# Performance work log

Hardware: AMD Instinct MI355X
Metric: run time of the kernel (lower is better)

The kernel has to match this reference:

```python
import jax, jax.numpy as jnp
import numpy as np

N_NODES = 50000
N_EDGES = 800000
IN_CH = 256
OUT_CH = 128
HID = 2 * OUT_CH  # 256
LN_EPS = 1e-5


def _add_self_loops(edge_index, n):
    loop = jnp.arange(n, dtype=edge_index.dtype)
    src = jnp.concatenate([edge_index[0], loop])
    dst = jnp.concatenate([edge_index[1], loop])
    return src, dst


def _gcn_norm(src, dst, n):
    # PyG GCNConv norm: deg over source index, symmetric normalization
    ones = jnp.ones(src.shape[0], dtype=jnp.float32)
    deg = jax.ops.segment_sum(ones, src, num_segments=n)
    dinv = jnp.where(deg > 0, deg ** -0.5, 0.0)
    return dinv[src] * dinv[dst]  # [E+N]


def _gcn_conv(x, src, dst, norm, w, b, gamma=None, beta=None):
    h = x @ w                              # [N, out]
    msgs = norm[:, None] * h[src]          # gather + scale, [E+N, out]
    out = jax.ops.segment_sum(msgs, dst, num_segments=x.shape[0])
    if gamma is not None:
        out = gamma * out + beta           # FiLM modulation (per-feature)
    return out + b


def _layernorm(x):
    mu = jnp.mean(x, axis=-1, keepdims=True)
    var = jnp.var(x, axis=-1, keepdims=True)
    return (x - mu) * jax.lax.rsqrt(var + LN_EPS)


def setup_inputs() -> dict:
    key = jax.random.key(0)
    ks = jax.random.split(key, 20)

    def g(k, shape, scale=0.05):
        return jax.random.normal(k, shape, dtype=jnp.float32) * scale

    x = jax.random.normal(ks[0], (N_NODES, IN_CH), dtype=jnp.float32)
    edge_index = jax.random.randint(ks[1], (2, N_EDGES), 0, N_NODES, dtype=jnp.int64)
    return {
        "x": x,
        "edge_index": edge_index,
        "conv1_w": g(ks[2], (IN_CH, HID)),
        "conv1_b": g(ks[3], (HID,)),
        "conv2_w": g(ks[4], (HID, OUT_CH)),
        "conv2_b": g(ks[5], (OUT_CH,)),
        "sig_conv_w": g(ks[6], (IN_CH, HID)),
        "sig_conv_b": g(ks[7], (HID,)),
        "fc1_w": g(ks[8], (HID, HID)),
        "fc1_b": g(ks[9], (HID,)),
        "fc2_w": g(ks[10], (HID, HID)),
        "fc2_b": g(ks[11], (HID,)),
        "fc3_w": g(ks[12], (OUT_CH, HID)),
        "fc3_b": g(ks[13], (OUT_CH,)),
        "fc4_w": g(ks[14], (OUT_CH, HID)),
        "fc4_b": g(ks[15], (OUT_CH,)),
    }


def reference(x, edge_index, conv1_w, conv1_b, conv2_w, conv2_b,
              sig_conv_w, sig_conv_b, fc1_w, fc1_b, fc2_w, fc2_b,
              fc3_w, fc3_b, fc4_w, fc4_b):
    n = x.shape[0]
    src, dst = _add_self_loops(edge_index, n)
    norm = _gcn_norm(src, dst, n)

    # --- GraphSignature (use_gcn_sig=True) ---
    s = jax.nn.relu(_gcn_conv(x, src, dst, norm, sig_conv_w, sig_conv_b))
    s = s.sum(0)  # [HID]
    gamma1 = jnp.tanh(s @ fc1_w.T + fc1_b)  # [HID]
    beta1 = jnp.tanh(s @ fc2_w.T + fc2_b)   # [HID]
    gamma2 = jnp.tanh(s @ fc3_w.T + fc3_b)  # [OUT]
    beta2 = jnp.tanh(s @ fc4_w.T + fc4_b)   # [OUT]

    # inner_loop=True: signature outputs are detached
    gamma1, beta1, gamma2, beta2 = map(jax.lax.stop_gradient,
                                       (gamma1, beta1, gamma2, beta2))

    # --- Encoder (GAE) ---
    h = jax.nn.relu(_gcn_conv(x, src, dst, norm, conv1_w, conv1_b,
                              gamma=gamma1, beta=beta1))
    h = _layernorm(h)
    out = _gcn_conv(h, src, dst, norm, conv2_w, conv2_b,
                    gamma=gamma2, beta=beta2)
    out = _layernorm(out)
    return out
```

## Files before the change

kernel.cpp:

```cpp
#include <hip/hip_runtime.h>

typedef _Float16 f16;
typedef f16 f16x8 __attribute__((ext_vector_type(8)));
typedef float f32x4 __attribute__((ext_vector_type(4)));
typedef unsigned short u16;
typedef unsigned int u32;

#define IN_CH  256
#define HID    256
#define OUT_CH 128
#define LN_EPS 1e-5f
#define NSLOT  32
#define NR     4
#define NC     64
#define RS     12544
#define HT     512


__global__ __launch_bounds__(HT) void k_hist(const int* __restrict__ ei, int nE, int nN,
                                             int* __restrict__ hP) {
    __shared__ int h[RS];
    int r = blockIdx.x & (NR - 1), c = blockIdx.x >> 2;
    int rsz = (nN + NR - 1) / NR;
    int r0 = r * rsz;
    int sz = nN - r0; if (sz > rsz) sz = rsz;
    for (int i = threadIdx.x; i < sz; i += HT) h[i] = 0;
    __syncthreads();
    int nT = nE + nN;
    int chunk = (nT + NC - 1) / NC;
    int e0 = c * chunk, e1 = e0 + chunk; if (e1 > nT) e1 = nT;
    for (int eb = e0 + (int)threadIdx.x; eb < e1; eb += HT * 4) {
        int ss[4], dd[4];
        #pragma unroll
        for (int u = 0; u < 4; u++) {
            int e = eb + u * HT;
            ss[u] = -1; dd[u] = -1;
            if (e < e1) {
                if (e < nE) { ss[u] = ei[e]; dd[u] = ei[nE + e]; }
                else { ss[u] = e - nE; dd[u] = e - nE; }
            }
        }
        #pragma unroll
        for (int u = 0; u < 4; u++) {
            if ((unsigned)(ss[u] - r0) < (unsigned)sz) atomicAdd(&h[ss[u] - r0], 1);
            if ((unsigned)(dd[u] - r0) < (unsigned)sz) atomicAdd(&h[dd[u] - r0], 0x10000);
        }
    }
    __syncthreads();
    for (int i = threadIdx.x; i < sz; i += HT) hP[(size_t)c * nN + r0 + i] = h[i];
}


__global__ __launch_bounds__(256) void k_alloc(const int* __restrict__ hP,
                                               int* __restrict__ rowstart,
                                               int* __restrict__ chunkbase,
                                               int* __restrict__ cnt_tot,
                                               float* __restrict__ dinv,
                                               int* __restrict__ ctr, int nN,
                                               const float* __restrict__ x, f16* __restrict__ xh,
                                               int nelem, int nAllocB, int nCast,
                                               const float* __restrict__ sigw,
                                               const float* __restrict__ c1w,
                                               const float* __restrict__ c2w,
                                               f16* __restrict__ Wt1, f16* __restrict__ Wt2) {
    int bid = blockIdx.x;
    if (bid < nAllocB) {
        int i = bid * 256 + threadIdx.x;
        int lane = threadIdx.x & 63;
        int cnt = 0, dg = 0;
        if (i < nN) {
            for (int c = 0; c < NC; c++) {
                unsigned pk = (unsigned)hP[(size_t)c * nN + i];
                cnt += (int)(pk >> 16);
                dg  += (int)(pk & 0xffffu);
            }
        }
        int p = cnt;
        #pragma unroll
        for (int off = 1; off < 64; off <<= 1) {
            int v = __shfl_up(p, off, 64);
            if (lane >= off) p += v;
        }
        int tot = __shfl(p, 63, 64);
        int base = 0;
        if (lane == 0) base = atomicAdd(ctr, tot);
        base = __shfl(base, 0, 64);
        if (i < nN) {
            int nb = base + p - cnt;
            rowstart[i] = nb;
            cnt_tot[i] = cnt;
            dinv[i] = rsqrtf((float)dg);
            int run = nb;
            for (int c = 0; c < NC; c++) {
                chunkbase[(size_t)c * nN + i] = run;
                run += (int)((unsigned)hP[(size_t)c * nN + i] >> 16);
            }
        }
    } else if (bid < nAllocB + nCast) {
        int i = (bid - nAllocB) * 2048 + threadIdx.x * 8;
        if (i >= nelem) return;
        float4 a = *(const float4*)(x + i);
        float4 b = *(const float4*)(x + i + 4);
        f16x8 o = { (f16)a.x, (f16)a.y, (f16)a.z, (f16)a.w,
                    (f16)b.x, (f16)b.y, (f16)b.z, (f16)b.w };
        *(f16x8*)(xh + i) = o;
    } else {
        int i = (bid - nAllocB - nCast) * 256 + threadIdx.x;
        if (i < 512 * 256) {
            int n = i >> 8, k = i & 255;
            float v = (n < 256) ? sigw[k * 256 + n] : c1w[k * 256 + (n - 256)];
            Wt1[(size_t)n * 256 + k] = (f16)v;
        } else {
            int j = i - 512 * 256;
            if (j < 128 * 256) {
                int n = j >> 8, k = j & 255;
                Wt2[(size_t)n * 256 + k] = (f16)c2w[k * 128 + n];
            }
        }
    }
}


__global__ __launch_bounds__(HT) void k_fill(const int* __restrict__ ei, int nE, int nN,
                                             const int* __restrict__ chunkbase,
                                             u16* __restrict__ src_sorted) {
    __shared__ int pos_[RS];
    int r = blockIdx.x & (NR - 1), c = blockIdx.x >> 2;
    int rsz = (nN + NR - 1) / NR;
    int r0 = r * rsz;
    int sz = nN - r0; if (sz > rsz) sz = rsz;
    for (int i = threadIdx.x; i < sz; i += HT)
        pos_[i] = chunkbase[(size_t)c * nN + r0 + i];
    __syncthreads();
    int nT = nE + nN;
    int chunk = (nT + NC - 1) / NC;
    int e0 = c * chunk, e1 = e0 + chunk; if (e1 > nT) e1 = nT;
    for (int eb = e0 + (int)threadIdx.x; eb < e1; eb += HT * 4) {
        int ss[4], dd[4];
        #pragma unroll
        for (int u = 0; u < 4; u++) {
            int e = eb + u * HT;
            ss[u] = -1; dd[u] = -1;
            if (e < e1) {
                if (e < nE) { ss[u] = ei[e]; dd[u] = ei[nE + e]; }
                else { ss[u] = e - nE; dd[u] = e - nE; }
            }
        }
        #pragma unroll
        for (int u = 0; u < 4; u++) {
            int l = dd[u] - r0;
            if ((unsigned)l < (unsigned)sz) {
                int pos = atomicAdd(&pos_[l], 1);
                src_sorted[pos] = (u16)ss[u];
            }
        }
    }
}


__global__ __launch_bounds__(256) void k_aggX(const f16* __restrict__ xh,
                                              const int* __restrict__ rowstart,
                                              const int* __restrict__ counts,
                                              const u16* __restrict__ srcs,
                                              const float* __restrict__ dinv,
                                              f16* __restrict__ AX, int nN) {
    int wv = threadIdx.x >> 6;
    int lane = threadIdx.x & 63;
    int node = blockIdx.x * 4 + wv;
    if (node >= nN) return;
    int h = lane >> 5, sub = lane & 31;
    int beg = rowstart[node];
    int cnt = counts[node];
    float acc0[8] = {}, acc1[8] = {};
    for (int base = 0; base < cnt; base += 64) {
        int el = base + lane;
        int sv = 0; float dv = 0.f;
        if (el < cnt) { sv = srcs[beg + el]; dv = dinv[sv]; }
        int rem = cnt - base; if (rem > 64) rem = 64;
        for (int e = 0; e < rem; e += 8) {
            int i0 = e + h, i1 = e + 2 + h, i2 = e + 4 + h, i3 = e + 6 + h;
            int sa = __shfl(sv, i0, 64), sb = __shfl(sv, i1, 64);
            int sc = __shfl(sv, i2, 64), sd = __shfl(sv, i3, 64);
            float na = __shfl(dv, i0, 64), nb = __shfl(dv, i1, 64);
            float nc = __shfl(dv, i2, 64), nd = __shfl(dv, i3, 64);
            if (i0 >= rem) na = 0.f;
            if (i1 >= rem) nb = 0.f;
            if (i2 >= rem) nc = 0.f;
            if (i3 >= rem) nd = 0.f;
            f16x8 va = *(const f16x8*)(xh + (size_t)sa * 256 + sub * 8);
            f16x8 vb = *(const f16x8*)(xh + (size_t)sb * 256 + sub * 8);
            f16x8 vc = *(const f16x8*)(xh + (size_t)sc * 256 + sub * 8);
            f16x8 vd = *(const f16x8*)(xh + (size_t)sd * 256 + sub * 8);
            #pragma unroll
            for (int j = 0; j < 8; j++) {
                acc0[j] = fmaf(na, (float)va[j], acc0[j]);
                acc1[j] = fmaf(nb, (float)vb[j], acc1[j]);
                acc0[j] = fmaf(nc, (float)vc[j], acc0[j]);
                acc1[j] = fmaf(nd, (float)vd[j], acc1[j]);
            }
        }
    }
    float dn = dinv[node];
    #pragma unroll
    for (int j = 0; j < 8; j++) {
        acc0[j] += acc1[j];
        acc0[j] += __shfl_xor(acc0[j], 32, 64);
    }
    if (lane < 32) {
        f16x8 o;
        #pragma unroll
        for (int j = 0; j < 8; j++) o[j] = (f16)(acc0[j] * dn);
        *(f16x8*)(AX + (size_t)node * 256 + sub * 8) = o;
    }
}


__global__ __launch_bounds__(256) void k_gemm_sig(const f16* __restrict__ AX,
                                                  const f16* __restrict__ Wt,
                                                  const float* __restrict__ sigb,
                                                  float* __restrict__ sig_part, int M) {
    __shared__ f16 tile[32][264];
    int t = threadIdx.x;
    int w = t >> 6, lane = t & 63, quad = lane >> 4, l16 = lane & 15;
    int m0 = blockIdx.x * 32;
    int cb = w * 64;
    f32x4 acc[2][4] = {};
    for (int kk = 0; kk < 256; kk += 32) {
        int ka = kk + quad * 8;
        f16x8 a[2];
        #pragma unroll
        for (int ms = 0; ms < 2; ms++) {
            int row = m0 + ms * 16 + l16; if (row >= M) row = M - 1;
            a[ms] = *(const f16x8*)(AX + (size_t)row * 256 + ka);
        }
        #pragma unroll
        for (int ns = 0; ns < 4; ns++) {
            f16x8 b = *(const f16x8*)(Wt + (size_t)(cb + ns * 16 + l16) * 256 + ka);
            acc[0][ns] = __builtin_amdgcn_mfma_f32_16x16x32_f16(a[0], b, acc[0][ns], 0, 0, 0);
            acc[1][ns] = __builtin_amdgcn_mfma_f32_16x16x32_f16(a[1], b, acc[1][ns], 0, 0, 0);
        }
    }
    #pragma unroll
    for (int ms = 0; ms < 2; ms++)
        #pragma unroll
        for (int ns = 0; ns < 4; ns++)
            #pragma unroll
            for (int r = 0; r < 4; r++) {
                int mr = ms * 16 + quad * 4 + r;
                int c = cb + ns * 16 + l16;
                float v = fmaxf(acc[ms][ns][r] + sigb[c], 0.f);
                if (m0 + mr >= M) v = 0.f;
                tile[mr][c] = (f16)v;
            }
    __syncthreads();
    float s = 0.f;
    #pragma unroll 8
    for (int r = 0; r < 32; r++) s += (float)tile[r][t];
    atomicAdd(&sig_part[(blockIdx.x & (NSLOT - 1)) * 256 + t], s);
}


__global__ __launch_bounds__(256) void k_fc(const float* __restrict__ sig_part,
                                            const float* __restrict__ f1w, const float* __restrict__ f1b,
                                            const float* __restrict__ f2w, const float* __restrict__ f2b,
                                            const float* __restrict__ f3w, const float* __restrict__ f3b,
                                            const float* __restrict__ f4w, const float* __restrict__ f4b,
                                            const float* __restrict__ c1b, const float* __restrict__ c2b,
                                            float* __restrict__ g1, float* __restrict__ bc1,
                                            float* __restrict__ g2, float* __restrict__ bc2) {
    __shared__ float ss[256];
    int t = threadIdx.x;
    float s = 0.f;
    for (int k = 0; k < NSLOT; k++) s += sig_part[k * 256 + t];
    ss[t] = s;
    __syncthreads();
    int wv = t >> 6, lane = t & 63;
    float s0 = ss[lane], s1 = ss[lane + 64], s2v = ss[lane + 128], s3 = ss[lane + 192];
    #pragma unroll
    for (int rr = 0; rr < 16; rr++) {
        int row = blockIdx.x * 64 + wv * 16 + rr;
        const float* w; const float* bb; const float* ex; float* dst; int r;
        if (row < 256)      { w = f1w; bb = f1b; dst = g1;  ex = 0;   r = row; }
        else if (row < 512) { w = f2w; bb = f2b; dst = bc1; ex = c1b; r = row - 256; }
        else if (row < 640) { w = f3w; bb = f3b; dst = g2;  ex = 0;   r = row - 512; }
        else                { w = f4w; bb = f4b; dst = bc2; ex = c2b; r = row - 640; }
        const float* wr = w + (size_t)r * 256;
        float a = wr[lane] * s0;
        a = fmaf(wr[lane + 64], s1, a);
        a = fmaf(wr[lane + 128], s2v, a);
        a = fmaf(wr[lane + 192], s3, a);
        #pragma unroll
        for (int off = 1; off < 64; off <<= 1) a += __shfl_xor(a, off, 64);
        if (lane == 0) dst[r] = tanhf(a + bb[r]) + (ex ? ex[r] : 0.f);
    }
}


__global__ __launch_bounds__(256) void k_c1f(const f16* __restrict__ AX,
                                             const f16* __restrict__ Wt,
                                             const f16* __restrict__ Wt2,
                                             const float* __restrict__ g1,
                                             const float* __restrict__ bc1,
                                             const float* __restrict__ dinv,
                                             f16* __restrict__ HW, int M) {
    __shared__ f16 ht[32][264];
    __shared__ float ps[32][5], ps2[32][5];
    __shared__ float mu_[32], rr_[32], sdinv[32];
    int t = threadIdx.x;
    int w = t >> 6, lane = t & 63, quad = lane >> 4, l16 = lane & 15;
    int m0 = blockIdx.x * 32;
    int cb = w * 64;
    f32x4 acc[2][4] = {};
    for (int kk = 0; kk < 256; kk += 32) {
        int ka = kk + quad * 8;
        f16x8 a[2];
        #pragma unroll
        for (int ms = 0; ms < 2; ms++) {
            int row = m0 + ms * 16 + l16; if (row >= M) row = M - 1;
            a[ms] = *(const f16x8*)(AX + (size_t)row * 256 + ka);
        }
        #pragma unroll
        for (int ns = 0; ns < 4; ns++) {
            f16x8 b = *(const f16x8*)(Wt + (size_t)(cb + ns * 16 + l16) * 256 + ka);
            acc[0][ns] = __builtin_amdgcn_mfma_f32_16x16x32_f16(a[0], b, acc[0][ns], 0, 0, 0);
            acc[1][ns] = __builtin_amdgcn_mfma_f32_16x16x32_f16(a[1], b, acc[1][ns], 0, 0, 0);
        }
    }

    float rs[2][4] = {{0.f,0.f,0.f,0.f},{0.f,0.f,0.f,0.f}};
    float rs2[2][4] = {{0.f,0.f,0.f,0.f},{0.f,0.f,0.f,0.f}};
    #pragma unroll
    for (int ns = 0; ns < 4; ns++) {
        int c = cb + ns * 16 + l16;
        float gv = g1[c], bv = bc1[c];
        #pragma unroll
        for (int ms = 0; ms < 2; ms++)
            #pragma unroll
            for (int r = 0; r < 4; r++) {
                float v = fmaxf(fmaf(gv, acc[ms][ns][r], bv), 0.f);
                acc[ms][ns][r] = v;
                rs[ms][r] += v;
                rs2[ms][r] = fmaf(v, v, rs2[ms][r]);
            }
    }
    #pragma unroll
    for (int off = 1; off < 16; off <<= 1)
        #pragma unroll
        for (int ms = 0; ms < 2; ms++)
            #pragma unroll
            for (int r = 0; r < 4; r++) {
                rs[ms][r]  += __shfl_xor(rs[ms][r], off, 64);
                rs2[ms][r] += __shfl_xor(rs2[ms][r], off, 64);
            }
    if (l16 == 0) {
        #pragma unroll
        for (int ms = 0; ms < 2; ms++)
            #pragma unroll
            for (int r = 0; r < 4; r++) {
                int mr = ms * 16 + quad * 4 + r;
                ps[mr][w] = rs[ms][r];
                ps2[mr][w] = rs2[ms][r];
            }
    }
    __syncthreads();
    if (t < 32) {
        float S = ps[t][0] + ps[t][1] + ps[t][2] + ps[t][3];
        float S2 = ps2[t][0] + ps2[t][1] + ps2[t][2] + ps2[t][3];
        float mu = S * (1.f / 256.f);
        mu_[t] = mu;
        rr_[t] = rsqrtf(S2 * (1.f / 256.f) - mu * mu + LN_EPS);
        int m = m0 + t;
        sdinv[t] = (m < M) ? dinv[m] : 0.f;
    }
    __syncthreads();
    #pragma unroll
    for (int ms = 0; ms < 2; ms++)
        #pragma unroll
        for (int r = 0; r < 4; r++) {
            int mr = ms * 16 + quad * 4 + r;
            float mu = mu_[mr], rr = rr_[mr];
            #pragma unroll
            for (int ns = 0; ns < 4; ns++)
                ht[mr][cb + ns * 16 + l16] = (f16)((acc[ms][ns][r] - mu) * rr);
        }
    __syncthreads();
    int cb2 = w * 32;
    f32x4 acc2[2][2] = {};
    for (int kk = 0; kk < 256; kk += 32) {
        int ka = kk + quad * 8;
        f16x8 a[2];
        #pragma unroll
        for (int ms = 0; ms < 2; ms++)
            a[ms] = *(const f16x8*)(&ht[ms * 16 + l16][ka]);
        #pragma unroll
        for (int ns = 0; ns < 2; ns++) {
            f16x8 b = *(const f16x8*)(Wt2 + (size_t)(cb2 + ns * 16 + l16) * 256 + ka);
            acc2[0][ns] = __builtin_amdgcn_mfma_f32_16x16x32_f16(a[0], b, acc2[0][ns], 0, 0, 0);
            acc2[1][ns] = __builtin_amdgcn_mfma_f32_16x16x32_f16(a[1], b, acc2[1][ns], 0, 0, 0);
        }
    }
    #pragma unroll
    for (int ms = 0; ms < 2; ms++)
        #pragma unroll
        for (int ns = 0; ns < 2; ns++)
            #pragma unroll
            for (int r = 0; r < 4; r++) {
                int mr = ms * 16 + quad * 4 + r;
                int m = m0 + mr;
                if (m < M) HW[(size_t)m * 128 + cb2 + ns * 16 + l16] = (f16)(acc2[ms][ns][r] * sdinv[mr]);
            }
}


__global__ __launch_bounds__(256) void k_agg2(const f16* __restrict__ HW,
                                              const int* __restrict__ rowstart,
                                              const int* __restrict__ counts,
                                              const u16* __restrict__ srcs,
                                              const float* __restrict__ dinv,
                                              const float* __restrict__ g2,
                                              const float* __restrict__ bc2,
                                              float* __restrict__ out, int nN) {
    int wv = threadIdx.x >> 6;
    int lane = threadIdx.x & 63;
    int node = blockIdx.x * 4 + wv;
    if (node >= nN) return;
    int q = lane >> 4, sub = lane & 15;
    int beg = rowstart[node];
    int cnt = counts[node];
    float acc0[8] = {}, acc1[8] = {};
    for (int base = 0; base < cnt; base += 64) {
        int el = base + lane;
        int sv = 0; float dv = 0.f;
        if (el < cnt) { sv = srcs[beg + el]; dv = 1.f; }
        int rem = cnt - base; if (rem > 64) rem = 64;
        for (int e = 0; e < rem; e += 8) {
            int i0 = e + q, i1 = e + 4 + q;
            int sa = __shfl(sv, i0, 64), sb = __shfl(sv, i1, 64);
            float na = __shfl(dv, i0, 64), nb = __shfl(dv, i1, 64);
            if (i0 >= rem) na = 0.f;
            if (i1 >= rem) nb = 0.f;
            f16x8 va = *(const f16x8*)(HW + (size_t)sa * 128 + sub * 8);
            f16x8 vb = *(const f16x8*)(HW + (size_t)sb * 128 + sub * 8);
            #pragma unroll
            for (int j = 0; j < 8; j++) {
                acc0[j] = fmaf(na, (float)va[j], acc0[j]);
                acc1[j] = fmaf(nb, (float)vb[j], acc1[j]);
            }
        }
    }
    float dn = dinv[node];
    #pragma unroll
    for (int j = 0; j < 8; j++) {
        acc0[j] += acc1[j];
        acc0[j] += __shfl_xor(acc0[j], 16, 64);
        acc0[j] += __shfl_xor(acc0[j], 32, 64);
    }
    int ch = sub * 8;
    float vfin[8];
    float s = 0.f, s2 = 0.f;
    #pragma unroll
    for (int j = 0; j < 8; j++) {
        float v = fmaf(g2[ch + j], acc0[j] * dn, bc2[ch + j]);
        vfin[j] = v;
        s += v; s2 = fmaf(v, v, s2);
    }
    #pragma unroll
    for (int off = 1; off < 16; off <<= 1) {
        s += __shfl_xor(s, off, 64);
        s2 += __shfl_xor(s2, off, 64);
    }
    float mu = s * (1.f / 128.f);
    float rr = rsqrtf(s2 * (1.f / 128.f) - mu * mu + LN_EPS);
    if (q == 0) {
        float4 o0 = { (vfin[0] - mu) * rr, (vfin[1] - mu) * rr,
                      (vfin[2] - mu) * rr, (vfin[3] - mu) * rr };
        float4 o1 = { (vfin[4] - mu) * rr, (vfin[5] - mu) * rr,
                      (vfin[6] - mu) * rr, (vfin[7] - mu) * rr };
        float* dst = out + (size_t)node * 128 + ch;
        *(float4*)dst = o0;
        *(float4*)(dst + 4) = o1;
    }
}


extern "C" void kernel_launch(void* const* d_in, const int* in_sizes, int n_in,
                              void* d_out, int out_size, void* d_ws, size_t ws_size,
                              hipStream_t stream) {
    const float* x    = (const float*)d_in[0];
    const int*   ei   = (const int*)d_in[1];
    const float* c1w  = (const float*)d_in[2];
    const float* c1b  = (const float*)d_in[3];
    const float* c2w  = (const float*)d_in[4];
    const float* c2b  = (const float*)d_in[5];
    const float* sigw = (const float*)d_in[6];
    const float* sigb = (const float*)d_in[7];
    const float* f1w  = (const float*)d_in[8];
    const float* f1b  = (const float*)d_in[9];
    const float* f2w  = (const float*)d_in[10];
    const float* f2b  = (const float*)d_in[11];
    const float* f3w  = (const float*)d_in[12];
    const float* f3b  = (const float*)d_in[13];
    const float* f4w  = (const float*)d_in[14];
    const float* f4b  = (const float*)d_in[15];
    float* out = (float*)d_out;

    int nN = in_sizes[0] / IN_CH;
    int nE = in_sizes[1] / 2;
    int nT = nE + nN;

    char* base = (char*)d_ws;
    size_t off = 0;
    auto alloc = [&](size_t bytes) { size_t o = off; off += (bytes + 255) & ~(size_t)255; return o; };

    size_t o_spart  = alloc((size_t)NSLOT * 256 * 4);
    size_t o_ctr    = alloc(256);
    size_t zero_bytes = off;
    size_t o_hP     = alloc((size_t)NC * nN * 4);
    size_t o_cbase  = alloc((size_t)NC * nN * 4);
    size_t o_g1     = alloc(256 * 4);
    size_t o_b1     = alloc(256 * 4);
    size_t o_g2     = alloc(128 * 4);
    size_t o_b2     = alloc(128 * 4);
    size_t o_rowst  = alloc((size_t)nN * 4);
    size_t o_cntt   = alloc((size_t)nN * 4);
    size_t o_dinv   = alloc((size_t)nN * 4);
    size_t o_src    = alloc((size_t)nT * 2);
    size_t o_wt1    = alloc(512 * 256 * 2);
    size_t o_wt2    = alloc(128 * 256 * 2);
    size_t o_xh     = alloc((size_t)nN * 256 * 2);
    size_t o_AX     = alloc((size_t)nN * 256 * 2);
    size_t o_HW     = alloc((size_t)nN * 128 * 2);

    float* spart  = (float*)(base + o_spart);
    int*   ctr    = (int*)(base + o_ctr);
    int*   hP     = (int*)(base + o_hP);
    int*   cbase  = (int*)(base + o_cbase);
    float* g1     = (float*)(base + o_g1);
    float* bc1    = (float*)(base + o_b1);
    float* g2     = (float*)(base + o_g2);
    float* bc2    = (float*)(base + o_b2);
    int*   rowst  = (int*)(base + o_rowst);
    int*   cntt   = (int*)(base + o_cntt);
    float* dinv   = (float*)(base + o_dinv);
    u16*   srcs   = (u16*)(base + o_src);
    f16*   Wt1    = (f16*)(base + o_wt1);
    f16*   Wt2    = (f16*)(base + o_wt2);
    f16*   xh     = (f16*)(base + o_xh);
    f16*   AX     = (f16*)(base + o_AX);
    f16*   HW     = (f16*)(base + o_HW);

    hipMemsetAsync(base, 0, zero_bytes, stream);

    k_hist<<<NR * NC, HT, 0, stream>>>(ei, nE, nN, hP);

    int nAllocB = (nN + 255) / 256;
    int nCast = (nN * IN_CH + 2047) / 2048;
    int nPrep = (512 * 256 + 128 * 256) / 256;
    k_alloc<<<nAllocB + nCast + nPrep, 256, 0, stream>>>(hP, rowst, cbase, cntt, dinv, ctr, nN,
                                                         x, xh, nN * IN_CH, nAllocB, nCast,
                                                         sigw, c1w, c2w, Wt1, Wt2);

    k_fill<<<NR * NC, HT, 0, stream>>>(ei, nE, nN, cbase, srcs);

    int nb4 = (nN + 3) / 4;
    int mg = (nN + 31) / 32;
    k_aggX<<<nb4, 256, 0, stream>>>(xh, rowst, cntt, srcs, dinv, AX, nN);
    k_gemm_sig<<<mg, 256, 0, stream>>>(AX, Wt1, sigb, spart, nN);
    k_fc<<<12, 256, 0, stream>>>(spart, f1w, f1b, f2w, f2b, f3w, f3b, f4w, f4b,
                                 c1b, c2b, g1, bc1, g2, bc2);
    k_c1f<<<mg, 256, 0, stream>>>(AX, Wt1 + 256 * 256, Wt2, g1, bc1, dinv, HW, nN);
    k_agg2<<<nb4, 256, 0, stream>>>(HW, rowst, cntt, srcs, dinv, g2, bc2, out, nN);
}
```

Baseline: 365.1 us.

## Pre-swizzle GEMM weights into MFMA fragment order and unroll gather loops deeper

Weight prep now stores the transposed f16 weights in MFMA B-fragment order, so each lane's 16-byte B load in the three GEMM kernels reads one contiguous, coalesced chunk instead of strided rows. The prep grid shrinks because each thread now writes eight values. The two aggregation kernels gain a 16-edge main loop that issues eight (or four) independent row gathers before accumulating, which raises memory-level parallelism at the cost of more registers. The old 8-edge loop remains as the tail.

```diff
diff --git a/kernel.cpp b/kernel.cpp
--- a/kernel.cpp
+++ b/kernel.cpp
@@ -106,16 +106,32 @@
         *(f16x8*)(xh + i) = o;
     } else {
         int i = (bid - nAllocB - nCast) * 256 + threadIdx.x;
-        if (i < 512 * 256) {
-            int n = i >> 8, k = i & 255;
-            float v = (n < 256) ? sigw[k * 256 + n] : c1w[k * 256 + (n - 256)];
-            Wt1[(size_t)n * 256 + k] = (f16)v;
+        if (i < 16384) {
+            int ct = i >> 9;
+            int rem = i & 511;
+            int kx = rem >> 6;
+            int lane = rem & 63;
+            int q = lane >> 4, l = lane & 15;
+            int n = (ct & 15) * 16 + l;
+            int k0 = kx * 32 + q * 8;
+            const float* src = (ct < 16) ? sigw : c1w;
+            f16x8 o;
+            #pragma unroll
+            for (int j = 0; j < 8; j++) o[j] = (f16)src[(size_t)(k0 + j) * 256 + n];
+            *(f16x8*)(Wt1 + (size_t)i * 8) = o;
         } else {
-            int j = i - 512 * 256;
-            if (j < 128 * 256) {
-                int n = j >> 8, k = j & 255;
-                Wt2[(size_t)n * 256 + k] = (f16)c2w[k * 128 + n];
-            }
+            int h = i - 16384;
+            int ct = h >> 9;
+            int rem = h & 511;
+            int kx = rem >> 6;
+            int lane = rem & 63;
+            int q = lane >> 4, l = lane & 15;
+            int n = ct * 16 + l;
+            int k0 = kx * 32 + q * 8;
+            f16x8 o;
+            #pragma unroll
+            for (int j = 0; j < 8; j++) o[j] = (f16)c2w[(size_t)(k0 + j) * 128 + n];
+            *(f16x8*)(Wt2 + (size_t)h * 8) = o;
         }
     }
 }
@@ -177,7 +193,28 @@
         int sv = 0; float dv = 0.f;
         if (el < cnt) { sv = srcs[beg + el]; dv = dinv[sv]; }
         int rem = cnt - base; if (rem > 64) rem = 64;
-        for (int e = 0; e < rem; e += 8) {
+        int e = 0;
+        for (; e + 16 <= rem; e += 16) {
+            int s_[8]; float n_[8];
+            #pragma unroll
+            for (int u = 0; u < 8; u++) {
+                int ii = e + u * 2 + h;
+                s_[u] = __shfl(sv, ii, 64);
+                n_[u] = __shfl(dv, ii, 64);
+            }
+            f16x8 v_[8];
+            #pragma unroll
+            for (int u = 0; u < 8; u++)
+                v_[u] = *(const f16x8*)(xh + (size_t)s_[u] * 256 + sub * 8);
+            #pragma unroll
+            for (int u = 0; u < 8; u++)
+                #pragma unroll
+                for (int j = 0; j < 8; j++) {
+                    float* a = (u & 1) ? acc1 : acc0;
+                    a[j] = fmaf(n_[u], (float)v_[u][j], a[j]);
+                }
+        }
+        for (; e < rem; e += 8) {
             int i0 = e + h, i1 = e + 2 + h, i2 = e + 4 + h, i3 = e + 6 + h;
             int sa = __shfl(sv, i0, 64), sb = __shfl(sv, i1, 64);
             int sc = __shfl(sv, i2, 64), sd = __shfl(sv, i3, 64);
@@ -225,8 +262,8 @@
     int m0 = blockIdx.x * 32;
     int cb = w * 64;
     f32x4 acc[2][4] = {};
-    for (int kk = 0; kk < 256; kk += 32) {
-        int ka = kk + quad * 8;
+    for (int kx = 0; kx < 8; kx++) {
+        int ka = kx * 32 + quad * 8;
         f16x8 a[2];
         #pragma unroll
         for (int ms = 0; ms < 2; ms++) {
@@ -235,7 +272,8 @@
         }
         #pragma unroll
         for (int ns = 0; ns < 4; ns++) {
-            f16x8 b = *(const f16x8*)(Wt + (size_t)(cb + ns * 16 + l16) * 256 + ka);
+            int ct = w * 4 + ns;
+            f16x8 b = *(const f16x8*)(Wt + ((size_t)((ct * 8 + kx) * 64 + lane) << 3));
             acc[0][ns] = __builtin_amdgcn_mfma_f32_16x16x32_f16(a[0], b, acc[0][ns], 0, 0, 0);
             acc[1][ns] = __builtin_amdgcn_mfma_f32_16x16x32_f16(a[1], b, acc[1][ns], 0, 0, 0);
         }
@@ -311,8 +349,8 @@
     int m0 = blockIdx.x * 32;
     int cb = w * 64;
     f32x4 acc[2][4] = {};
-    for (int kk = 0; kk < 256; kk += 32) {
-        int ka = kk + quad * 8;
+    for (int kx = 0; kx < 8; kx++) {
+        int ka = kx * 32 + quad * 8;
         f16x8 a[2];
         #pragma unroll
         for (int ms = 0; ms < 2; ms++) {
@@ -321,7 +359,8 @@
         }
         #pragma unroll
         for (int ns = 0; ns < 4; ns++) {
-            f16x8 b = *(const f16x8*)(Wt + (size_t)(cb + ns * 16 + l16) * 256 + ka);
+            int ct = w * 4 + ns;
+            f16x8 b = *(const f16x8*)(Wt + ((size_t)((ct * 8 + kx) * 64 + lane) << 3));
             acc[0][ns] = __builtin_amdgcn_mfma_f32_16x16x32_f16(a[0], b, acc[0][ns], 0, 0, 0);
             acc[1][ns] = __builtin_amdgcn_mfma_f32_16x16x32_f16(a[1], b, acc[1][ns], 0, 0, 0);
         }
@@ -386,15 +425,16 @@
     __syncthreads();
     int cb2 = w * 32;
     f32x4 acc2[2][2] = {};
-    for (int kk = 0; kk < 256; kk += 32) {
-        int ka = kk + quad * 8;
+    for (int kx = 0; kx < 8; kx++) {
+        int ka = kx * 32 + quad * 8;
         f16x8 a[2];
         #pragma unroll
         for (int ms = 0; ms < 2; ms++)
             a[ms] = *(const f16x8*)(&ht[ms * 16 + l16][ka]);
         #pragma unroll
         for (int ns = 0; ns < 2; ns++) {
-            f16x8 b = *(const f16x8*)(Wt2 + (size_t)(cb2 + ns * 16 + l16) * 256 + ka);
+            int ct = w * 2 + ns;
+            f16x8 b = *(const f16x8*)(Wt2 + ((size_t)((ct * 8 + kx) * 64 + lane) << 3));
             acc2[0][ns] = __builtin_amdgcn_mfma_f32_16x16x32_f16(a[0], b, acc2[0][ns], 0, 0, 0);
             acc2[1][ns] = __builtin_amdgcn_mfma_f32_16x16x32_f16(a[1], b, acc2[1][ns], 0, 0, 0);
         }
@@ -433,7 +473,28 @@
         int sv = 0; float dv = 0.f;
         if (el < cnt) { sv = srcs[beg + el]; dv = 1.f; }
         int rem = cnt - base; if (rem > 64) rem = 64;
-        for (int e = 0; e < rem; e += 8) {
+        int e = 0;
+        for (; e + 16 <= rem; e += 16) {
+            int s_[4]; float n_[4];
+            #pragma unroll
+            for (int u = 0; u < 4; u++) {
+                int ii = e + u * 4 + q;
+                s_[u] = __shfl(sv, ii, 64);
+                n_[u] = __shfl(dv, ii, 64);
+            }
+            f16x8 v_[4];
+            #pragma unroll
+            for (int u = 0; u < 4; u++)
+                v_[u] = *(const f16x8*)(HW + (size_t)s_[u] * 128 + sub * 8);
+            #pragma unroll
+            for (int u = 0; u < 4; u++)
+                #pragma unroll
+                for (int j = 0; j < 8; j++) {
+                    float* a = (u & 1) ? acc1 : acc0;
+                    a[j] = fmaf(n_[u], (float)v_[u][j], a[j]);
+                }
+        }
+        for (; e < rem; e += 8) {
             int i0 = e + q, i1 = e + 4 + q;
             int sa = __shfl(sv, i0, 64), sb = __shfl(sv, i1, 64);
             float na = __shfl(dv, i0, 64), nb = __shfl(dv, i1, 64);
@@ -555,7 +616,7 @@
 
     int nAllocB = (nN + 255) / 256;
     int nCast = (nN * IN_CH + 2047) / 2048;
-    int nPrep = (512 * 256 + 128 * 256) / 256;
+    int nPrep = (512 * 256 + 128 * 256) / 2048;
     k_alloc<<<nAllocB + nCast + nPrep, 256, 0, stream>>>(hP, rowst, cbase, cntt, dinv, ctr, nN,
                                                          x, xh, nN * IN_CH, nAllocB, nCast,
                                                          sigw, c1w, c2w, Wt1, Wt2);
```

Result: faster. 331.9 us (-9.1%).
